# Performance work log

Hardware: AMD Instinct MI355X
Metric: run time of the kernel (lower is better)

Reference implementation:

```python
import jax, jax.numpy as jnp
import numpy as np

B, H, L, TAU, THETA = 8192, 256, 4, 8, 8


def setup_inputs() -> dict:
    key = jax.random.key(0)
    ks = jax.random.split(key, 16)
    w = lambda k, shape: (jax.random.normal(k, shape, jnp.float32) * 0.02)
    return {
        "x": jax.random.normal(ks[0], (B, H), jnp.float32),
        "t_att": jax.random.normal(ks[1], (L, TAU, B, H), jnp.float32),
        "s_att": jax.random.normal(ks[2], (L, TAU, B, H), jnp.float32),
        "embed_w": w(ks[3], (H, H)),
        "embed_b": jnp.zeros((H,), jnp.float32),
        "wtn": w(ks[4], (L, H, H)),
        "btn": jnp.zeros((L, H), jnp.float32),
        "wsn": w(ks[5], (L, H, H)),
        "bsn": jnp.zeros((L, H), jnp.float32),
        "wt": w(ks[6], (L, 3 * H, H)),
        "bt": jnp.zeros((L, 3 * H), jnp.float32),
        "ws": w(ks[7], (L, 3 * H, H)),
        "bs": jnp.zeros((L, 3 * H), jnp.float32),
        "out_w": w(ks[8], (H, H)),
        "out_b": jnp.zeros((H,), jnp.float32),
    }


def _forward(x, t_att, s_att, embed_w, embed_b, wtn, btn, wsn, bsn, wt, bt, ws, bs, out_w, out_b):
    n_layers, tau = t_att.shape[0], t_att.shape[1]
    b, h = x.shape
    scale = 1.0 / np.sqrt(h).astype(np.float32)
    theta = THETA

    S = x @ embed_w.T + embed_b  # embed: [B, H]
    # rolling spatial buffers, start as theta zero entries
    t_sp = jnp.zeros((theta, b, h), x.dtype)
    s_sp = jnp.zeros((theta, b, h), x.dtype)

    for i in range(n_layers):
        T_last = t_att[i, -1]  # [B, H]
        # append current S_t / last T_t to spatial buffers, keep last theta
        s_sp = jnp.concatenate([s_sp[1:], S[None]], axis=0)
        t_sp = jnp.concatenate([t_sp[1:], T_last[None]], axis=0)
        # s_att[i].append(S_t); slice last tau -> keys include current S
        s_keys = jnp.concatenate([s_att[i, 1:], S[None]], axis=0)  # [tau, B, H]
        t_vals = t_att[i]  # [tau, B, H]

        s_next = S @ wsn[i].T + bsn[i]
        t_next = T_last @ wtn[i].T + btn[i]

        # temporal attention over last-tau history
        w_t = jax.nn.softmax(jnp.einsum('kbh,bh->kb', s_keys, s_next) * scale, axis=0)
        T_trend = jnp.einsum('kb,kbh->bh', w_t, t_vals)
        t_gate = jax.nn.sigmoid(t_next)
        T_fusion = T_last * t_gate + (1.0 - t_gate) * T_trend

        # spatial attention over last-theta buffer
        w_s = jax.nn.softmax(jnp.einsum('kbh,bh->kb', t_sp, t_next) * scale, axis=0)
        S_trend = jnp.einsum('kb,kbh->bh', w_s, s_sp)
        s_gate = jax.nn.sigmoid(s_next)
        S_fusion = S * s_gate + (1.0 - s_gate) * S_trend

        Tc = T_fusion @ wt[i].T + bt[i]  # [B, 3H]
        Sc = S_fusion @ ws[i].T + bs[i]
        t_g, t_t_, t_s_ = jnp.split(Tc, 3, axis=-1)
        s_g, s_t_, s_s_ = jnp.split(Sc, 3, axis=-1)
        Tg = jax.nn.sigmoid(t_g)
        Sg = jax.nn.sigmoid(s_g)
        # T_new feeds the (stateful) history; S carries to next layer
        S = Sg * s_s_ + (1.0 - Sg) * t_s_

    return jnp.tanh(S @ out_w.T + out_b)


def reference(x, t_att, s_att, embed_w, embed_b, wtn, btn, wsn, bsn, wt, bt, ws, bs, out_w, out_b):
    return _forward(x, t_att, s_att, embed_w, embed_b, wtn, btn, wsn, bsn, wt, bt, ws, bs, out_w, out_b)
```

## Files before the change

kernel.cpp:

```cpp
#include <hip/hip_runtime.h>
#include <cmath>

typedef __attribute__((ext_vector_type(8))) short short8;
typedef __attribute__((ext_vector_type(4))) float f32x4;
typedef __attribute__((ext_vector_type(4))) unsigned short us4;
typedef unsigned short u16;

#define BATCH 8192
#define HDIM  256
static constexpr size_t BH = (size_t)BATCH * HDIM;

__device__ __forceinline__ u16 f2bf(float f) {
    union { float f; unsigned u; } v; v.f = f;
    unsigned r = v.u + 0x7FFFu + ((v.u >> 16) & 1u);
    return (u16)(r >> 16);
}
__device__ __forceinline__ float bf2f(u16 u) {
    union { unsigned u; float f; } v; v.u = ((unsigned)u) << 16;
    return v.f;
}
__device__ __forceinline__ float sigmoidf_(float x) {
    return 1.f / (1.f + __expf(-x));
}
__device__ __forceinline__ short8 cvt8(const float* p) {
    f32x4 lo = *(const f32x4*)p, hi = *(const f32x4*)(p + 4);
    short8 t;
    t[0] = (short)f2bf(lo[0]); t[1] = (short)f2bf(lo[1]);
    t[2] = (short)f2bf(lo[2]); t[3] = (short)f2bf(lo[3]);
    t[4] = (short)f2bf(hi[0]); t[5] = (short)f2bf(hi[1]);
    t[6] = (short)f2bf(hi[2]); t[7] = (short)f2bf(hi[3]);
    return t;
}
__device__ __forceinline__ float dot4(const f32x4& a, const float* b) {
    return a[0] * b[0] + a[1] * b[1] + a[2] * b[2] + a[3] * b[3];
}

__global__ __launch_bounds__(256) void convert_weights(
    const float* __restrict__ embed_w, const float* __restrict__ wtn,
    const float* __restrict__ wsn, const float* __restrict__ wt,
    const float* __restrict__ ws, const float* __restrict__ out_w,
    u16* __restrict__ dst)
{
    int idx = blockIdx.x * 256 + threadIdx.x;
    int e = idx * 4;
    if (e >= 22 * 65536) return;
    int c = e >> 16, o = e & 65535;
    const float* src;
    if (c == 0)      src = embed_w + o;
    else if (c < 5)  src = wtn + (size_t)(c - 1) * 65536 + o;
    else if (c < 9)  src = wsn + (size_t)(c - 5) * 65536 + o;
    else if (c < 13) src = wt + (size_t)(c - 9) * 768 * 256 + 512 * 256 + o;
    else if (c < 17) src = ws + (size_t)(c - 13) * 768 * 256 + o;
    else if (c < 21) src = ws + (size_t)(c - 17) * 768 * 256 + 512 * 256 + o;
    else             src = out_w + o;
    f32x4 v = *(const f32x4*)src;
    us4 r;
#pragma unroll
    for (int j = 0; j < 4; ++j) r[j] = f2bf(v[j]);
    *(us4*)(dst + e) = r;
}

#define PAD 264
__global__ __launch_bounds__(256, 2) void stau_mega(
    const float* __restrict__ x,
    const float* __restrict__ t_att, const float* __restrict__ s_att,
    const u16* __restrict__ Wbf,
    const float* __restrict__ embed_b,
    const float* __restrict__ btn, const float* __restrict__ bsn,
    const float* __restrict__ bt, const float* __restrict__ bs,
    const float* __restrict__ out_b,
    float* __restrict__ outp)
{
    __shared__ __align__(16) u16 S_lds[5][16][PAD];
    __shared__ __align__(16) u16 sn_lds[16][PAD];
    __shared__ __align__(16) u16 tn_lds[16][PAD];
    __shared__ __align__(16) u16 tf_lds[16][PAD];
    __shared__ __align__(16) u16 sf_lds[16][PAD];

    const int lane = threadIdx.x & 63;
    const int wave = threadIdx.x >> 6;
    const int lr = lane & 15;
    const int kg = lane >> 4;
    const int row0 = blockIdx.x * 16;
    const float scale = 0.0625f;

    {
        const int n0 = wave * 64;
        f32x4 acc[4] = {};
        for (int k0 = 0; k0 < 256; k0 += 32) {
            int k = k0 + kg * 8;
            short8 a = cvt8(x + (size_t)(row0 + lr) * 256 + k);
#pragma unroll
            for (int nf = 0; nf < 4; ++nf) {
                short8 b = *(const short8*)(Wbf + (size_t)(n0 + nf * 16 + lr) * 256 + k);
                acc[nf] = __builtin_amdgcn_mfma_f32_16x16x32_bf16(a, b, acc[nf], 0, 0, 0);
            }
        }
#pragma unroll
        for (int nf = 0; nf < 4; ++nf) {
            int n = n0 + nf * 16 + lr;
            float bn = embed_b[n];
#pragma unroll
            for (int r = 0; r < 4; ++r)
                S_lds[0][kg * 4 + r][n] = f2bf(acc[nf][r] + bn);
        }
    }
    __syncthreads();

    for (int i = 0; i < 4; ++i) {
        {
            const int g = wave >> 1;
            const int n0 = (wave & 1) * 128;
            const u16* Wm = Wbf + (size_t)((g ? 1 : 5) + i) * 65536;
            const float* bias = (g ? btn : bsn) + i * 256;
            f32x4 acc[8] = {};
            for (int k0 = 0; k0 < 256; k0 += 32) {
                int k = k0 + kg * 8;
                short8 a;
                if (g == 0) a = *(const short8*)(&S_lds[i][lr][k]);
                else        a = cvt8(t_att + ((size_t)i * 8 + 7) * BH + (size_t)(row0 + lr) * 256 + k);
#pragma unroll
                for (int nf = 0; nf < 8; ++nf) {
                    short8 b = *(const short8*)(Wm + (size_t)(n0 + nf * 16 + lr) * 256 + k);
                    acc[nf] = __builtin_amdgcn_mfma_f32_16x16x32_bf16(a, b, acc[nf], 0, 0, 0);
                }
            }
            u16 (*dst)[PAD] = g ? tn_lds : sn_lds;
#pragma unroll
            for (int nf = 0; nf < 8; ++nf) {
                int n = n0 + nf * 16 + lr;
                float bn = bias[n];
#pragma unroll
                for (int r = 0; r < 4; ++r)
                    dst[kg * 4 + r][n] = f2bf(acc[nf][r] + bn);
            }
        }
        __syncthreads();

        for (int rr = wave * 4; rr < wave * 4 + 4; ++rr) {
            const size_t ro = (size_t)(row0 + rr) * 256 + lane * 4;
            const float* sa = s_att + (size_t)i * 8 * BH + ro;
            const float* ta = t_att + (size_t)i * 8 * BH + ro;

            f32x4 sav[7], tav[8], tspv[3] = {};
#pragma unroll
            for (int kk = 0; kk < 7; ++kk) sav[kk] = *(const f32x4*)(sa + (size_t)(kk + 1) * BH);
#pragma unroll
            for (int kk = 0; kk < 8; ++kk) tav[kk] = *(const f32x4*)(ta + (size_t)kk * BH);
#pragma unroll
            for (int jj = 0; jj < 3; ++jj)
                if (jj < i) tspv[jj] = *(const f32x4*)(t_att + ((size_t)jj * 8 + 7) * BH + ro);

            us4 snu = *(const us4*)&sn_lds[rr][lane * 4];
            us4 tnu = *(const us4*)&tn_lds[rr][lane * 4];
            us4 scu = *(const us4*)&S_lds[i][rr][lane * 4];
            float sn[4], tn[4], Sc[4];
#pragma unroll
            for (int j = 0; j < 4; ++j) { sn[j] = bf2f(snu[j]); tn[j] = bf2f(tnu[j]); Sc[j] = bf2f(scu[j]); }

            float v[12];
#pragma unroll
            for (int kk = 0; kk < 7; ++kk) v[kk] = dot4(sav[kk], sn);
            v[7] = Sc[0] * sn[0] + Sc[1] * sn[1] + Sc[2] * sn[2] + Sc[3] * sn[3];
#pragma unroll
            for (int jj = 0; jj < 3; ++jj) v[8 + jj] = (jj < i) ? dot4(tspv[jj], tn) : 0.f;
            v[11] = dot4(tav[7], tn);

#pragma unroll
            for (int o = 32; o > 0; o >>= 1)
#pragma unroll
                for (int u = 0; u < 12; ++u) v[u] += __shfl_xor(v[u], o);

            float m = v[0] * scale;
#pragma unroll
            for (int kk = 1; kk < 8; ++kk) m = fmaxf(m, v[kk] * scale);
            float w8[8], den = 0.f;
#pragma unroll
            for (int kk = 0; kk < 8; ++kk) { w8[kk] = __expf(v[kk] * scale - m); den += w8[kk]; }
            float inv = 1.f / den;

            float Tt[4] = {0.f, 0.f, 0.f, 0.f};
#pragma unroll
            for (int kk = 0; kk < 8; ++kk)
#pragma unroll
                for (int j = 0; j < 4; ++j) Tt[j] += w8[kk] * tav[kk][j];
            us4 ot;
#pragma unroll
            for (int j = 0; j < 4; ++j) {
                float g = sigmoidf_(tn[j]);
                ot[j] = f2bf(tav[7][j] * g + (1.f - g) * Tt[j] * inv);
            }
            *(us4*)&tf_lds[rr][lane * 4] = ot;

            float ms = fmaxf(0.f, v[11] * scale);
#pragma unroll
            for (int jj = 0; jj < 3; ++jj)
                if (jj < i) ms = fmaxf(ms, v[8 + jj] * scale);
            float dens = (float)(7 - i) * __expf(-ms);
            float St[4];
            {
                float w = __expf(v[11] * scale - ms);
                dens += w;
#pragma unroll
                for (int j = 0; j < 4; ++j) St[j] = w * Sc[j];
            }
#pragma unroll
            for (int jj = 0; jj < 3; ++jj)
                if (jj < i) {
                    float w = __expf(v[8 + jj] * scale - ms);
                    dens += w;
                    us4 shu = *(const us4*)&S_lds[jj][rr][lane * 4];
#pragma unroll
                    for (int j = 0; j < 4; ++j) St[j] += w * bf2f(shu[j]);
                }
            float invs = 1.f / dens;
            us4 os;
#pragma unroll
            for (int j = 0; j < 4; ++j) {
                float g = sigmoidf_(sn[j]);
                os[j] = f2bf(Sc[j] * g + (1.f - g) * St[j] * invs);
            }
            *(us4*)&sf_lds[rr][lane * 4] = os;
        }
        __syncthreads();

        {
            const int n0 = wave * 64;
            const u16* Wt3 = Wbf + (size_t)(9  + i) * 65536;
            const u16* Ws1 = Wbf + (size_t)(13 + i) * 65536;
            const u16* Ws3 = Wbf + (size_t)(17 + i) * 65536;
            f32x4 aT[4] = {}, aG[4] = {}, aS[4] = {};
            for (int k0 = 0; k0 < 256; k0 += 32) {
                int k = k0 + kg * 8;
                short8 at = *(const short8*)(&tf_lds[lr][k]);
                short8 as = *(const short8*)(&sf_lds[lr][k]);
#pragma unroll
                for (int nf = 0; nf < 4; ++nf) {
                    size_t wo = (size_t)(n0 + nf * 16 + lr) * 256 + k;
                    aT[nf] = __builtin_amdgcn_mfma_f32_16x16x32_bf16(at, *(const short8*)(Wt3 + wo), aT[nf], 0, 0, 0);
                    aG[nf] = __builtin_amdgcn_mfma_f32_16x16x32_bf16(as, *(const short8*)(Ws1 + wo), aG[nf], 0, 0, 0);
                    aS[nf] = __builtin_amdgcn_mfma_f32_16x16x32_bf16(as, *(const short8*)(Ws3 + wo), aS[nf], 0, 0, 0);
                }
            }
            const float* b1 = bt + i * 768 + 512;
            const float* b2 = bs + i * 768;
            const float* b3 = bs + i * 768 + 512;
#pragma unroll
            for (int nf = 0; nf < 4; ++nf) {
                int n = n0 + nf * 16 + lr;
                float bb1 = b1[n], bb2 = b2[n], bb3 = b3[n];
#pragma unroll
                for (int r = 0; r < 4; ++r) {
                    float gv = sigmoidf_(aG[nf][r] + bb2);
                    float vv = gv * (aS[nf][r] + bb3) + (1.f - gv) * (aT[nf][r] + bb1);
                    S_lds[i + 1][kg * 4 + r][n] = f2bf(vv);
                }
            }
        }
        __syncthreads();
    }

    {
        const int n0 = wave * 64;
        const u16* Wo = Wbf + (size_t)21 * 65536;
        f32x4 acc[4] = {};
        for (int k0 = 0; k0 < 256; k0 += 32) {
            int k = k0 + kg * 8;
            short8 a = *(const short8*)(&S_lds[4][lr][k]);
#pragma unroll
            for (int nf = 0; nf < 4; ++nf) {
                short8 b = *(const short8*)(Wo + (size_t)(n0 + nf * 16 + lr) * 256 + k);
                acc[nf] = __builtin_amdgcn_mfma_f32_16x16x32_bf16(a, b, acc[nf], 0, 0, 0);
            }
        }
#pragma unroll
        for (int nf = 0; nf < 4; ++nf) {
            int n = n0 + nf * 16 + lr;
            float bn = out_b[n];
#pragma unroll
            for (int r = 0; r < 4; ++r)
                outp[(size_t)(row0 + kg * 4 + r) * 256 + n] = tanhf(acc[nf][r] + bn);
        }
    }
}

extern "C" void kernel_launch(void* const* d_in, const int* in_sizes, int n_in,
                              void* d_out, int out_size, void* d_ws, size_t ws_size,
                              hipStream_t stream)
{
    (void)in_sizes; (void)n_in; (void)out_size; (void)ws_size;
    const float* x       = (const float*)d_in[0];
    const float* t_att   = (const float*)d_in[1];
    const float* s_att   = (const float*)d_in[2];
    const float* embed_w = (const float*)d_in[3];
    const float* embed_b = (const float*)d_in[4];
    const float* wtn     = (const float*)d_in[5];
    const float* btn     = (const float*)d_in[6];
    const float* wsn     = (const float*)d_in[7];
    const float* bsn     = (const float*)d_in[8];
    const float* wt      = (const float*)d_in[9];
    const float* bt      = (const float*)d_in[10];
    const float* ws_in   = (const float*)d_in[11];
    const float* bs      = (const float*)d_in[12];
    const float* out_w   = (const float*)d_in[13];
    const float* out_b   = (const float*)d_in[14];

    u16* Wbf = (u16*)d_ws;

    convert_weights<<<1408, 256, 0, stream>>>(embed_w, wtn, wsn, wt, ws_in, out_w, Wbf);

    stau_mega<<<BATCH / 16, 256, 0, stream>>>(
        x, t_att, s_att, Wbf, embed_b, btn, bsn, bt, bs, out_b, (float*)d_out);
}
```

Measured before the change: 278.3 us.

## Split fused megakernel into per-layer attention and GEMM kernels via global intermediates

```diff
diff --git a/kernel.cpp b/kernel.cpp
--- a/kernel.cpp
+++ b/kernel.cpp
@@ -7,8 +7,8 @@
 typedef unsigned short u16;
 
 #define BATCH 8192
-#define HDIM  256
-static constexpr size_t BH = (size_t)BATCH * HDIM;
+static constexpr size_t BH = (size_t)BATCH * 256;
+#define LPAD 264
 
 __device__ __forceinline__ u16 f2bf(float f) {
     union { float f; unsigned u; } v; v.f = f;
@@ -60,36 +60,37 @@
     *(us4*)(dst + e) = r;
 }
 
-#define PAD 264
-__global__ __launch_bounds__(256, 2) void stau_mega(
-    const float* __restrict__ x,
-    const float* __restrict__ t_att, const float* __restrict__ s_att,
+__global__ __launch_bounds__(256, 4) void embed_dual(
+    const float* __restrict__ x, const float* __restrict__ t_att,
     const u16* __restrict__ Wbf,
     const float* __restrict__ embed_b,
     const float* __restrict__ btn, const float* __restrict__ bsn,
-    const float* __restrict__ bt, const float* __restrict__ bs,
-    const float* __restrict__ out_b,
-    float* __restrict__ outp)
+    u16* __restrict__ S_hist, u16* __restrict__ sn_g, u16* __restrict__ tn_g)
 {
-    __shared__ __align__(16) u16 S_lds[5][16][PAD];
-    __shared__ __align__(16) u16 sn_lds[16][PAD];
-    __shared__ __align__(16) u16 tn_lds[16][PAD];
-    __shared__ __align__(16) u16 tf_lds[16][PAD];
-    __shared__ __align__(16) u16 sf_lds[16][PAD];
-
-    const int lane = threadIdx.x & 63;
-    const int wave = threadIdx.x >> 6;
-    const int lr = lane & 15;
-    const int kg = lane >> 4;
+    __shared__ __align__(16) u16 Ax[16][LPAD];
+    __shared__ __align__(16) u16 Tn[16][LPAD];
+    __shared__ __align__(16) u16 S0[16][LPAD];
+    const int t = threadIdx.x;
     const int row0 = blockIdx.x * 16;
-    const float scale = 0.0625f;
-
-    {
-        const int n0 = wave * 64;
+    {
+        int r = t >> 4, c0 = (t & 15) * 16;
+        const float* px = x + (size_t)(row0 + r) * 256 + c0;
+        const float* pt = t_att + (size_t)7 * BH + (size_t)(row0 + r) * 256 + c0;
+        *(short8*)&Ax[r][c0]     = cvt8(px);
+        *(short8*)&Ax[r][c0 + 8] = cvt8(px + 8);
+        *(short8*)&Tn[r][c0]     = cvt8(pt);
+        *(short8*)&Tn[r][c0 + 8] = cvt8(pt + 8);
+    }
+    __syncthreads();
+    const int lane = t & 63, wave = t >> 6;
+    const int lr = lane & 15, kg = lane >> 4;
+    const int n0 = wave * 64;
+
+    {
         f32x4 acc[4] = {};
         for (int k0 = 0; k0 < 256; k0 += 32) {
             int k = k0 + kg * 8;
-            short8 a = cvt8(x + (size_t)(row0 + lr) * 256 + k);
+            short8 a = *(const short8*)&Ax[lr][k];
 #pragma unroll
             for (int nf = 0; nf < 4; ++nf) {
                 short8 b = *(const short8*)(Wbf + (size_t)(n0 + nf * 16 + lr) * 256 + k);
@@ -101,172 +102,145 @@
             int n = n0 + nf * 16 + lr;
             float bn = embed_b[n];
 #pragma unroll
-            for (int r = 0; r < 4; ++r)
-                S_lds[0][kg * 4 + r][n] = f2bf(acc[nf][r] + bn);
+            for (int r = 0; r < 4; ++r) {
+                u16 bv = f2bf(acc[nf][r] + bn);
+                S_hist[(size_t)(row0 + kg * 4 + r) * 256 + n] = bv;
+                S0[kg * 4 + r][n] = bv;
+            }
         }
     }
     __syncthreads();
 
-    for (int i = 0; i < 4; ++i) {
-        {
-            const int g = wave >> 1;
-            const int n0 = (wave & 1) * 128;
-            const u16* Wm = Wbf + (size_t)((g ? 1 : 5) + i) * 65536;
-            const float* bias = (g ? btn : bsn) + i * 256;
-            f32x4 acc[8] = {};
-            for (int k0 = 0; k0 < 256; k0 += 32) {
-                int k = k0 + kg * 8;
-                short8 a;
-                if (g == 0) a = *(const short8*)(&S_lds[i][lr][k]);
-                else        a = cvt8(t_att + ((size_t)i * 8 + 7) * BH + (size_t)(row0 + lr) * 256 + k);
-#pragma unroll
-                for (int nf = 0; nf < 8; ++nf) {
-                    short8 b = *(const short8*)(Wm + (size_t)(n0 + nf * 16 + lr) * 256 + k);
-                    acc[nf] = __builtin_amdgcn_mfma_f32_16x16x32_bf16(a, b, acc[nf], 0, 0, 0);
-                }
-            }
-            u16 (*dst)[PAD] = g ? tn_lds : sn_lds;
-#pragma unroll
-            for (int nf = 0; nf < 8; ++nf) {
-                int n = n0 + nf * 16 + lr;
-                float bn = bias[n];
-#pragma unroll
-                for (int r = 0; r < 4; ++r)
-                    dst[kg * 4 + r][n] = f2bf(acc[nf][r] + bn);
-            }
-        }
-        __syncthreads();
-
-        for (int rr = wave * 4; rr < wave * 4 + 4; ++rr) {
-            const size_t ro = (size_t)(row0 + rr) * 256 + lane * 4;
-            const float* sa = s_att + (size_t)i * 8 * BH + ro;
-            const float* ta = t_att + (size_t)i * 8 * BH + ro;
-
-            f32x4 sav[7], tav[8], tspv[3] = {};
-#pragma unroll
-            for (int kk = 0; kk < 7; ++kk) sav[kk] = *(const f32x4*)(sa + (size_t)(kk + 1) * BH);
-#pragma unroll
-            for (int kk = 0; kk < 8; ++kk) tav[kk] = *(const f32x4*)(ta + (size_t)kk * BH);
-#pragma unroll
-            for (int jj = 0; jj < 3; ++jj)
-                if (jj < i) tspv[jj] = *(const f32x4*)(t_att + ((size_t)jj * 8 + 7) * BH + ro);
-
-            us4 snu = *(const us4*)&sn_lds[rr][lane * 4];
-            us4 tnu = *(const us4*)&tn_lds[rr][lane * 4];
-            us4 scu = *(const us4*)&S_lds[i][rr][lane * 4];
-            float sn[4], tn[4], Sc[4];
-#pragma unroll
-            for (int j = 0; j < 4; ++j) { sn[j] = bf2f(snu[j]); tn[j] = bf2f(tnu[j]); Sc[j] = bf2f(scu[j]); }
-
-            float v[12];
-#pragma unroll
-            for (int kk = 0; kk < 7; ++kk) v[kk] = dot4(sav[kk], sn);
-            v[7] = Sc[0] * sn[0] + Sc[1] * sn[1] + Sc[2] * sn[2] + Sc[3] * sn[3];
-#pragma unroll
-            for (int jj = 0; jj < 3; ++jj) v[8 + jj] = (jj < i) ? dot4(tspv[jj], tn) : 0.f;
-            v[11] = dot4(tav[7], tn);
-
-#pragma unroll
-            for (int o = 32; o > 0; o >>= 1)
-#pragma unroll
-                for (int u = 0; u < 12; ++u) v[u] += __shfl_xor(v[u], o);
-
-            float m = v[0] * scale;
-#pragma unroll
-            for (int kk = 1; kk < 8; ++kk) m = fmaxf(m, v[kk] * scale);
-            float w8[8], den = 0.f;
-#pragma unroll
-            for (int kk = 0; kk < 8; ++kk) { w8[kk] = __expf(v[kk] * scale - m); den += w8[kk]; }
-            float inv = 1.f / den;
-
-            float Tt[4] = {0.f, 0.f, 0.f, 0.f};
-#pragma unroll
-            for (int kk = 0; kk < 8; ++kk)
-#pragma unroll
-                for (int j = 0; j < 4; ++j) Tt[j] += w8[kk] * tav[kk][j];
-            us4 ot;
-#pragma unroll
-            for (int j = 0; j < 4; ++j) {
-                float g = sigmoidf_(tn[j]);
-                ot[j] = f2bf(tav[7][j] * g + (1.f - g) * Tt[j] * inv);
-            }
-            *(us4*)&tf_lds[rr][lane * 4] = ot;
-
-            float ms = fmaxf(0.f, v[11] * scale);
-#pragma unroll
-            for (int jj = 0; jj < 3; ++jj)
-                if (jj < i) ms = fmaxf(ms, v[8 + jj] * scale);
-            float dens = (float)(7 - i) * __expf(-ms);
-            float St[4];
-            {
-                float w = __expf(v[11] * scale - ms);
-                dens += w;
-#pragma unroll
-                for (int j = 0; j < 4; ++j) St[j] = w * Sc[j];
-            }
-#pragma unroll
-            for (int jj = 0; jj < 3; ++jj)
-                if (jj < i) {
-                    float w = __expf(v[8 + jj] * scale - ms);
-                    dens += w;
-                    us4 shu = *(const us4*)&S_lds[jj][rr][lane * 4];
-#pragma unroll
-                    for (int j = 0; j < 4; ++j) St[j] += w * bf2f(shu[j]);
-                }
-            float invs = 1.f / dens;
-            us4 os;
-#pragma unroll
-            for (int j = 0; j < 4; ++j) {
-                float g = sigmoidf_(sn[j]);
-                os[j] = f2bf(Sc[j] * g + (1.f - g) * St[j] * invs);
-            }
-            *(us4*)&sf_lds[rr][lane * 4] = os;
-        }
-        __syncthreads();
-
-        {
-            const int n0 = wave * 64;
-            const u16* Wt3 = Wbf + (size_t)(9  + i) * 65536;
-            const u16* Ws1 = Wbf + (size_t)(13 + i) * 65536;
-            const u16* Ws3 = Wbf + (size_t)(17 + i) * 65536;
-            f32x4 aT[4] = {}, aG[4] = {}, aS[4] = {};
-            for (int k0 = 0; k0 < 256; k0 += 32) {
-                int k = k0 + kg * 8;
-                short8 at = *(const short8*)(&tf_lds[lr][k]);
-                short8 as = *(const short8*)(&sf_lds[lr][k]);
-#pragma unroll
-                for (int nf = 0; nf < 4; ++nf) {
-                    size_t wo = (size_t)(n0 + nf * 16 + lr) * 256 + k;
-                    aT[nf] = __builtin_amdgcn_mfma_f32_16x16x32_bf16(at, *(const short8*)(Wt3 + wo), aT[nf], 0, 0, 0);
-                    aG[nf] = __builtin_amdgcn_mfma_f32_16x16x32_bf16(as, *(const short8*)(Ws1 + wo), aG[nf], 0, 0, 0);
-                    aS[nf] = __builtin_amdgcn_mfma_f32_16x16x32_bf16(as, *(const short8*)(Ws3 + wo), aS[nf], 0, 0, 0);
-                }
-            }
-            const float* b1 = bt + i * 768 + 512;
-            const float* b2 = bs + i * 768;
-            const float* b3 = bs + i * 768 + 512;
+    {
+        const u16* Wsn = Wbf + (size_t)5 * 65536;
+        const u16* Wtn = Wbf + (size_t)1 * 65536;
+        f32x4 aS[4] = {}, aT[4] = {};
+        for (int k0 = 0; k0 < 256; k0 += 32) {
+            int k = k0 + kg * 8;
+            short8 a1 = *(const short8*)&S0[lr][k];
+            short8 a2 = *(const short8*)&Tn[lr][k];
 #pragma unroll
             for (int nf = 0; nf < 4; ++nf) {
-                int n = n0 + nf * 16 + lr;
-                float bb1 = b1[n], bb2 = b2[n], bb3 = b3[n];
-#pragma unroll
-                for (int r = 0; r < 4; ++r) {
-                    float gv = sigmoidf_(aG[nf][r] + bb2);
-                    float vv = gv * (aS[nf][r] + bb3) + (1.f - gv) * (aT[nf][r] + bb1);
-                    S_lds[i + 1][kg * 4 + r][n] = f2bf(vv);
-                }
-            }
-        }
-        __syncthreads();
-    }
-
-    {
-        const int n0 = wave * 64;
+                size_t wo = (size_t)(n0 + nf * 16 + lr) * 256 + k;
+                aS[nf] = __builtin_amdgcn_mfma_f32_16x16x32_bf16(a1, *(const short8*)(Wsn + wo), aS[nf], 0, 0, 0);
+                aT[nf] = __builtin_amdgcn_mfma_f32_16x16x32_bf16(a2, *(const short8*)(Wtn + wo), aT[nf], 0, 0, 0);
+            }
+        }
+#pragma unroll
+        for (int nf = 0; nf < 4; ++nf) {
+            int n = n0 + nf * 16 + lr;
+            float bS = bsn[n], bT = btn[n];
+#pragma unroll
+            for (int r = 0; r < 4; ++r) {
+                sn_g[(size_t)(row0 + kg * 4 + r) * 256 + n] = f2bf(aS[nf][r] + bS);
+                tn_g[(size_t)(row0 + kg * 4 + r) * 256 + n] = f2bf(aT[nf][r] + bT);
+            }
+        }
+    }
+}
+
+template<int I, bool LAST>
+__global__ __launch_bounds__(256, 4) void triple_next(
+    const u16* __restrict__ tf_g, const u16* __restrict__ sf_g,
+    const float* __restrict__ t_att, const u16* __restrict__ Wbf,
+    const float* __restrict__ bt, const float* __restrict__ bs,
+    const float* __restrict__ btn, const float* __restrict__ bsn,
+    const float* __restrict__ out_b,
+    u16* __restrict__ S_hist, u16* __restrict__ sn_g, u16* __restrict__ tn_g,
+    float* __restrict__ outp)
+{
+    __shared__ __align__(16) u16 Tf[16][LPAD];
+    __shared__ __align__(16) u16 Sf[16][LPAD];
+    __shared__ __align__(16) u16 Sn[16][LPAD];
+    __shared__ __align__(16) u16 Tx[16][LPAD];
+    const int t = threadIdx.x;
+    const int row0 = blockIdx.x * 16;
+    {
+        int r = t >> 4, c0 = (t & 15) * 16;
+        size_t off = (size_t)(row0 + r) * 256 + c0;
+        *(short8*)&Tf[r][c0]     = *(const short8*)(tf_g + off);
+        *(short8*)&Tf[r][c0 + 8] = *(const short8*)(tf_g + off + 8);
+        *(short8*)&Sf[r][c0]     = *(const short8*)(sf_g + off);
+        *(short8*)&Sf[r][c0 + 8] = *(const short8*)(sf_g + off + 8);
+        if constexpr (!LAST) {
+            const float* pt = t_att + ((size_t)(I + 1) * 8 + 7) * BH + off;
+            *(short8*)&Tx[r][c0]     = cvt8(pt);
+            *(short8*)&Tx[r][c0 + 8] = cvt8(pt + 8);
+        }
+    }
+    __syncthreads();
+    const int lane = t & 63, wave = t >> 6;
+    const int lr = lane & 15, kg = lane >> 4;
+    const int n0 = wave * 64;
+
+    {
+        const u16* Wt3 = Wbf + (size_t)(9 + I) * 65536;
+        const u16* Ws1 = Wbf + (size_t)(13 + I) * 65536;
+        const u16* Ws3 = Wbf + (size_t)(17 + I) * 65536;
+        f32x4 aT[4] = {}, aG[4] = {}, aS[4] = {};
+        for (int k0 = 0; k0 < 256; k0 += 32) {
+            int k = k0 + kg * 8;
+            short8 at = *(const short8*)&Tf[lr][k];
+            short8 as = *(const short8*)&Sf[lr][k];
+#pragma unroll
+            for (int nf = 0; nf < 4; ++nf) {
+                size_t wo = (size_t)(n0 + nf * 16 + lr) * 256 + k;
+                aT[nf] = __builtin_amdgcn_mfma_f32_16x16x32_bf16(at, *(const short8*)(Wt3 + wo), aT[nf], 0, 0, 0);
+                aG[nf] = __builtin_amdgcn_mfma_f32_16x16x32_bf16(as, *(const short8*)(Ws1 + wo), aG[nf], 0, 0, 0);
+                aS[nf] = __builtin_amdgcn_mfma_f32_16x16x32_bf16(as, *(const short8*)(Ws3 + wo), aS[nf], 0, 0, 0);
+            }
+        }
+        const float* b1 = bt + I * 768 + 512;
+        const float* b2 = bs + I * 768;
+        const float* b3 = bs + I * 768 + 512;
+#pragma unroll
+        for (int nf = 0; nf < 4; ++nf) {
+            int n = n0 + nf * 16 + lr;
+            float bb1 = b1[n], bb2 = b2[n], bb3 = b3[n];
+#pragma unroll
+            for (int r = 0; r < 4; ++r) {
+                float gv = sigmoidf_(aG[nf][r] + bb2);
+                float v = gv * (aS[nf][r] + bb3) + (1.f - gv) * (aT[nf][r] + bb1);
+                u16 bv = f2bf(v);
+                Sn[kg * 4 + r][n] = bv;
+                if constexpr (!LAST)
+                    S_hist[(size_t)(I + 1) * BH + (size_t)(row0 + kg * 4 + r) * 256 + n] = bv;
+            }
+        }
+    }
+    __syncthreads();
+
+    if constexpr (!LAST) {
+        const u16* Wsn = Wbf + (size_t)(5 + I + 1) * 65536;
+        const u16* Wtn = Wbf + (size_t)(1 + I + 1) * 65536;
+        f32x4 aS[4] = {}, aT[4] = {};
+        for (int k0 = 0; k0 < 256; k0 += 32) {
+            int k = k0 + kg * 8;
+            short8 a1 = *(const short8*)&Sn[lr][k];
+            short8 a2 = *(const short8*)&Tx[lr][k];
+#pragma unroll
+            for (int nf = 0; nf < 4; ++nf) {
+                size_t wo = (size_t)(n0 + nf * 16 + lr) * 256 + k;
+                aS[nf] = __builtin_amdgcn_mfma_f32_16x16x32_bf16(a1, *(const short8*)(Wsn + wo), aS[nf], 0, 0, 0);
+                aT[nf] = __builtin_amdgcn_mfma_f32_16x16x32_bf16(a2, *(const short8*)(Wtn + wo), aT[nf], 0, 0, 0);
+            }
+        }
+#pragma unroll
+        for (int nf = 0; nf < 4; ++nf) {
+            int n = n0 + nf * 16 + lr;
+            float bS = bsn[(I + 1) * 256 + n], bT = btn[(I + 1) * 256 + n];
+#pragma unroll
+            for (int r = 0; r < 4; ++r) {
+                sn_g[(size_t)(row0 + kg * 4 + r) * 256 + n] = f2bf(aS[nf][r] + bS);
+                tn_g[(size_t)(row0 + kg * 4 + r) * 256 + n] = f2bf(aT[nf][r] + bT);
+            }
+        }
+    } else {
         const u16* Wo = Wbf + (size_t)21 * 65536;
         f32x4 acc[4] = {};
         for (int k0 = 0; k0 < 256; k0 += 32) {
             int k = k0 + kg * 8;
-            short8 a = *(const short8*)(&S_lds[4][lr][k]);
+            short8 a = *(const short8*)&Sn[lr][k];
 #pragma unroll
             for (int nf = 0; nf < 4; ++nf) {
                 short8 b = *(const short8*)(Wo + (size_t)(n0 + nf * 16 + lr) * 256 + k);
@@ -282,6 +256,103 @@
                 outp[(size_t)(row0 + kg * 4 + r) * 256 + n] = tanhf(acc[nf][r] + bn);
         }
     }
+}
+
+template<int I>
+__global__ __launch_bounds__(256) void attn_k(
+    const float* __restrict__ t_att, const float* __restrict__ s_att,
+    const u16* __restrict__ S_hist,
+    const u16* __restrict__ sn_g, const u16* __restrict__ tn_g,
+    u16* __restrict__ tf_g, u16* __restrict__ sf_g)
+{
+    const int lane = threadIdx.x & 63;
+    const int row = blockIdx.x * 4 + (threadIdx.x >> 6);
+    const size_t ro = (size_t)row * 256 + lane * 4;
+    const float scale = 0.0625f;
+
+    const float* sa = s_att + (size_t)I * 8 * BH + ro;
+    const float* ta = t_att + (size_t)I * 8 * BH + ro;
+
+    us4 snu = *(const us4*)(sn_g + ro);
+    us4 tnu = *(const us4*)(tn_g + ro);
+    us4 scu = *(const us4*)(S_hist + (size_t)I * BH + ro);
+    us4 shu[I > 0 ? I : 1];
+#pragma unroll
+    for (int jj = 0; jj < I; ++jj) shu[jj] = *(const us4*)(S_hist + (size_t)jj * BH + ro);
+
+    f32x4 sav[7], tav[8], tsp[I > 0 ? I : 1];
+#pragma unroll
+    for (int kk = 0; kk < 7; ++kk) sav[kk] = *(const f32x4*)(sa + (size_t)(kk + 1) * BH);
+#pragma unroll
+    for (int kk = 0; kk < 8; ++kk) tav[kk] = *(const f32x4*)(ta + (size_t)kk * BH);
+#pragma unroll
+    for (int jj = 0; jj < I; ++jj) tsp[jj] = *(const f32x4*)(t_att + ((size_t)jj * 8 + 7) * BH + ro);
+
+    float sn[4], tn[4], Sc[4];
+#pragma unroll
+    for (int j = 0; j < 4; ++j) { sn[j] = bf2f(snu[j]); tn[j] = bf2f(tnu[j]); Sc[j] = bf2f(scu[j]); }
+
+    constexpr int NV = 9 + I;
+    float v[NV];
+#pragma unroll
+    for (int kk = 0; kk < 7; ++kk) v[kk] = dot4(sav[kk], sn);
+    v[7] = Sc[0] * sn[0] + Sc[1] * sn[1] + Sc[2] * sn[2] + Sc[3] * sn[3];
+#pragma unroll
+    for (int jj = 0; jj < I; ++jj) v[8 + jj] = dot4(tsp[jj], tn);
+    v[8 + I] = dot4(tav[7], tn);
+
+#pragma unroll
+    for (int o = 32; o > 0; o >>= 1)
+#pragma unroll
+        for (int u = 0; u < NV; ++u) v[u] += __shfl_xor(v[u], o);
+
+    float m = v[0] * scale;
+#pragma unroll
+    for (int kk = 1; kk < 8; ++kk) m = fmaxf(m, v[kk] * scale);
+    float w8[8], den = 0.f;
+#pragma unroll
+    for (int kk = 0; kk < 8; ++kk) { w8[kk] = __expf(v[kk] * scale - m); den += w8[kk]; }
+    float inv = 1.f / den;
+
+    float Tt[4] = {0.f, 0.f, 0.f, 0.f};
+#pragma unroll
+    for (int kk = 0; kk < 8; ++kk)
+#pragma unroll
+        for (int j = 0; j < 4; ++j) Tt[j] += w8[kk] * tav[kk][j];
+    us4 ot;
+#pragma unroll
+    for (int j = 0; j < 4; ++j) {
+        float g = sigmoidf_(tn[j]);
+        ot[j] = f2bf(tav[7][j] * g + (1.f - g) * Tt[j] * inv);
+    }
+    *(us4*)(tf_g + ro) = ot;
+
+    float ms = fmaxf(0.f, v[8 + I] * scale);
+#pragma unroll
+    for (int jj = 0; jj < I; ++jj) ms = fmaxf(ms, v[8 + jj] * scale);
+    float dens = (float)(7 - I) * __expf(-ms);
+    float St[4];
+    {
+        float w = __expf(v[8 + I] * scale - ms);
+        dens += w;
+#pragma unroll
+        for (int j = 0; j < 4; ++j) St[j] = w * Sc[j];
+    }
+#pragma unroll
+    for (int jj = 0; jj < I; ++jj) {
+        float w = __expf(v[8 + jj] * scale - ms);
+        dens += w;
+#pragma unroll
+        for (int j = 0; j < 4; ++j) St[j] += w * bf2f(shu[jj][j]);
+    }
+    float invs = 1.f / dens;
+    us4 os;
+#pragma unroll
+    for (int j = 0; j < 4; ++j) {
+        float g = sigmoidf_(sn[j]);
+        os[j] = f2bf(Sc[j] * g + (1.f - g) * St[j] * invs);
+    }
+    *(us4*)(sf_g + ro) = os;
 }
 
 extern "C" void kernel_launch(void* const* d_in, const int* in_sizes, int n_in,
@@ -305,10 +376,32 @@
     const float* out_w   = (const float*)d_in[13];
     const float* out_b   = (const float*)d_in[14];
 
-    u16* Wbf = (u16*)d_ws;
+    u16* wsp    = (u16*)d_ws;
+    u16* Wbf    = wsp;
+    u16* S_hist = wsp + (size_t)22 * 65536;
+    u16* sn_g   = S_hist + 4 * BH;
+    u16* tn_g   = sn_g + BH;
+    u16* tf_g   = tn_g + BH;
+    u16* sf_g   = tf_g + BH;
 
     convert_weights<<<1408, 256, 0, stream>>>(embed_w, wtn, wsn, wt, ws_in, out_w, Wbf);
 
-    stau_mega<<<BATCH / 16, 256, 0, stream>>>(
-        x, t_att, s_att, Wbf, embed_b, btn, bsn, bt, bs, out_b, (float*)d_out);
-}
+    embed_dual<<<BATCH / 16, 256, 0, stream>>>(x, t_att, Wbf, embed_b, btn, bsn,
+                                               S_hist, sn_g, tn_g);
+
+    attn_k<0><<<BATCH / 4, 256, 0, stream>>>(t_att, s_att, S_hist, sn_g, tn_g, tf_g, sf_g);
+    triple_next<0, false><<<BATCH / 16, 256, 0, stream>>>(
+        tf_g, sf_g, t_att, Wbf, bt, bs, btn, bsn, out_b, S_hist, sn_g, tn_g, nullptr);
+
+    attn_k<1><<<BATCH / 4, 256, 0, stream>>>(t_att, s_att, S_hist, sn_g, tn_g, tf_g, sf_g);
+    triple_next<1, false><<<BATCH / 16, 256, 0, stream>>>(
+        tf_g, sf_g, t_att, Wbf, bt, bs, btn, bsn, out_b, S_hist, sn_g, tn_g, nullptr);
+
+    attn_k<2><<<BATCH / 4, 256, 0, stream>>>(t_att, s_att, S_hist, sn_g, tn_g, tf_g, sf_g);
+    triple_next<2, false><<<BATCH / 16, 256, 0, stream>>>(
+        tf_g, sf_g, t_att, Wbf, bt, bs, btn, bsn, out_b, S_hist, sn_g, tn_g, nullptr);
+
+    attn_k<3><<<BATCH / 4, 256, 0, stream>>>(t_att, s_att, S_hist, sn_g, tn_g, tf_g, sf_g);
+    triple_next<3, true><<<BATCH / 16, 256, 0, stream>>>(
+        tf_g, sf_g, t_att, Wbf, bt, bs, btn, bsn, out_b, S_hist, sn_g, tn_g, (float*)d_out);
+}
```

Result: slower. 336.5 us (+20.9%).
